# Optimization experiments

Hardware: AMD Instinct MI355X
Metric: run time of the kernel (lower is better)

The kernel has to match this reference:

```python
import jax, jax.numpy as jnp
import numpy as np
import math

B, S, H, NH, NKV, D, I, LCK = 2, 1024, 2048, 32, 8, 64, 8192, 3
EPS = 1e-6
THETA = 10000.0


def rms_norm(x, w, eps=EPS):
    xf = x.astype(jnp.float32)
    var = jnp.mean(xf * xf, axis=-1, keepdims=True)
    return (w * (xf * jax.lax.rsqrt(var + eps))).astype(x.dtype)


def rotate_half(x):
    d = x.shape[-1] // 2
    return jnp.concatenate([-x[..., d:], x[..., :d]], axis=-1)


def setup_inputs() -> dict:
    key = jax.random.key(0)
    ks = jax.random.split(key, 16)
    sc = 0.02
    inp = {
        'input_emb': jax.random.normal(ks[0], (B, S, H), jnp.float32),
        'hidden_states': jax.random.normal(ks[1], (B, S, H), jnp.float32),
        'cache_k': jax.random.normal(ks[2], (LCK, B, NH, S, D), jnp.float32),
        'cache_v': jax.random.normal(ks[3], (LCK, B, NH, S, D), jnp.float32),
    }
    neg = jnp.finfo(jnp.float32).min
    causal = jnp.where(jnp.tril(jnp.ones((S, S), bool)), 0.0, neg).astype(jnp.float32)
    inp['attention_mask'] = jnp.broadcast_to(causal[None, None], (B, 1, S, S))
    inp['position_ids'] = jnp.broadcast_to(jnp.arange(S, dtype=jnp.int32)[None], (B, S))
    inp['wq'] = jax.random.normal(ks[4], (NH * D, 2 * H), jnp.float32) * sc
    inp['wk'] = jax.random.normal(ks[5], (NKV * D, 2 * H), jnp.float32) * sc
    inp['wv'] = jax.random.normal(ks[6], (NKV * D, 2 * H), jnp.float32) * sc
    inp['wo'] = jax.random.normal(ks[7], (H, NH * D), jnp.float32) * sc
    inp['w_gate'] = jax.random.normal(ks[8], (I, H), jnp.float32) * sc
    inp['w_up'] = jax.random.normal(ks[9], (I, H), jnp.float32) * sc
    inp['w_down'] = jax.random.normal(ks[10], (H, I), jnp.float32) * sc
    inp['hidden_norm_w'] = jnp.ones((H,), jnp.float32)
    inp['input_ln_w'] = jnp.ones((H,), jnp.float32)
    inp['post_ln_w'] = jnp.ones((H,), jnp.float32)
    return inp


def _forward(input_emb, hidden_states, cache_k, cache_v, attention_mask, position_ids,
             wq, wk, wv, wo, w_gate, w_up, w_down, hidden_norm_w, input_ln_w, post_ln_w):
    residual = hidden_states
    h = rms_norm(hidden_states, hidden_norm_w)
    e = rms_norm(input_emb, input_ln_w)
    x = jnp.concatenate([e, h], axis=-1)  # [B,S,2H]

    q = jnp.einsum('bsi,oi->bso', x, wq).reshape(B, S, NH, D).transpose(0, 2, 1, 3)
    k = jnp.einsum('bsi,oi->bso', x, wk).reshape(B, S, NKV, D).transpose(0, 2, 1, 3)
    v = jnp.einsum('bsi,oi->bso', x, wv).reshape(B, S, NKV, D).transpose(0, 2, 1, 3)

    # RoPE table up to seq_len = S + LCK, indexed at position_ids + LCK
    inv_freq = 1.0 / (THETA ** (jnp.arange(0, D, 2, dtype=jnp.float32) / D))
    t = jnp.arange(S + LCK, dtype=jnp.float32)
    freqs = t[:, None] * inv_freq[None, :]
    emb = jnp.concatenate([freqs, freqs], axis=-1)  # [S+LCK, D]
    pos = position_ids + LCK
    cos = jnp.cos(emb)[pos][:, None]  # [B,1,S,D]
    sin = jnp.sin(emb)[pos][:, None]
    q = q * cos + rotate_half(q) * sin
    k = k * cos + rotate_half(k) * sin

    n_rep = NH // NKV
    k = jnp.repeat(k, n_rep, axis=1)  # [B,NH,S,D]
    v = jnp.repeat(v, n_rep, axis=1)

    scale = 1.0 / math.sqrt(D)
    # full causal attention against the oldest cache entry
    s0 = jnp.einsum('bhqd,bhkd->bhqk', q, cache_k[0]) * scale + attention_mask
    # diagonal (same-position) attention against remaining cache entries + current keys
    extra_k = jnp.concatenate([cache_k[1:], k[None]], axis=0)  # [LCK,B,NH,S,D]
    extra_v = jnp.concatenate([cache_v[1:], v[None]], axis=0)
    sd = jnp.einsum('bhqd,nbhqd->bhqn', q, extra_k) * scale  # [B,NH,S,LCK]

    attn = jax.nn.softmax(jnp.concatenate([s0, sd], axis=-1).astype(jnp.float32), axis=-1).astype(q.dtype)
    out = jnp.einsum('bhqk,bhkd->bhqd', attn[..., :S], cache_v[0])
    out = out + jnp.einsum('bhqn,nbhqd->bhqd', attn[..., S:], extra_v)
    out = out.transpose(0, 2, 1, 3).reshape(B, S, NH * D)
    attn_out = jnp.einsum('bsi,oi->bso', out, wo)

    h2 = residual + attn_out
    hn = rms_norm(h2, post_ln_w)
    mlp = jnp.einsum('bsi,oi->bso', jax.nn.silu(jnp.einsum('bsi,oi->bso', hn, w_gate)) * jnp.einsum('bsi,oi->bso', hn, w_up), w_down)
    return h2 + mlp


def reference(input_emb, hidden_states, cache_k, cache_v, attention_mask, position_ids,
              wq, wk, wv, wo, w_gate, w_up, w_down, hidden_norm_w, input_ln_w, post_ln_w):
    return _forward(input_emb, hidden_states, cache_k, cache_v, attention_mask, position_ids,
                    wq, wk, wv, wo, w_gate, w_up, w_down, hidden_norm_w, input_ln_w, post_ln_w)
```

## Files before the change

### kernel.cpp

```cpp
#include <hip/hip_runtime.h>
#include <math.h>

#define B_   2
#define S_   1024
#define H_   2048
#define NH_  32
#define NKV_ 8
#define D_   64
#define I_   8192
#define LCK_ 3
#define M_   (B_ * S_)

typedef unsigned short u16;
typedef unsigned int   u32;
typedef __attribute__((ext_vector_type(8))) short bf16x8;
typedef __attribute__((ext_vector_type(4))) float f32x4;
typedef __attribute__((ext_vector_type(2))) unsigned int u32x2;

__device__ __forceinline__ u16 f2b(float f) {
  u32 u = __float_as_uint(f);
  u += 0x7fffu + ((u >> 16) & 1u);
  return (u16)(u >> 16);
}
__device__ __forceinline__ float b2f(u16 h) { return __uint_as_float(((u32)h) << 16); }

__device__ __forceinline__ void st_bf4(u16* p, float a, float b, float c, float d) {
  u32x2 v;
  v.x = (u32)f2b(a) | ((u32)f2b(b) << 16);
  v.y = (u32)f2b(c) | ((u32)f2b(d) << 16);
  *(u32x2*)p = v;
}

__device__ __forceinline__ void cvt16(const float4& a, const float4& b,
                                      const float4& c, const float4& d,
                                      bf16x8& lo, bf16x8& hi) {
  lo[0] = (short)f2b(a.x); lo[1] = (short)f2b(a.y); lo[2] = (short)f2b(a.z); lo[3] = (short)f2b(a.w);
  lo[4] = (short)f2b(b.x); lo[5] = (short)f2b(b.y); lo[6] = (short)f2b(b.z); lo[7] = (short)f2b(b.w);
  hi[0] = (short)f2b(c.x); hi[1] = (short)f2b(c.y); hi[2] = (short)f2b(c.z); hi[3] = (short)f2b(c.w);
  hi[4] = (short)f2b(d.x); hi[5] = (short)f2b(d.y); hi[6] = (short)f2b(d.z); hi[7] = (short)f2b(d.w);
}

__device__ __forceinline__ void async16(const void* g, void* l) {
  __builtin_amdgcn_global_load_lds(
      (const __attribute__((address_space(1))) unsigned int*)(uintptr_t)g,
      (__attribute__((address_space(3))) unsigned int*)(unsigned int)(uintptr_t)l,
      16, 0, 0);
}

__global__ __launch_bounds__(256) void norm_concat_kernel(
    const float* __restrict__ emb, const float* __restrict__ hid,
    const float* __restrict__ w_e, const float* __restrict__ w_h,
    u16* __restrict__ x)
{
  const int row = blockIdx.x;
  const int t = threadIdx.x;
  const float* e = emb + (size_t)row * H_;
  const float* h = hid + (size_t)row * H_;

  const float4 ev0 = *(const float4*)&e[t * 4];
  const float4 ev1 = *(const float4*)&e[t * 4 + 1024];
  const float4 hv0 = *(const float4*)&h[t * 4];
  const float4 hv1 = *(const float4*)&h[t * 4 + 1024];

  float se = ev0.x*ev0.x + ev0.y*ev0.y + ev0.z*ev0.z + ev0.w*ev0.w
           + ev1.x*ev1.x + ev1.y*ev1.y + ev1.z*ev1.z + ev1.w*ev1.w;
  float sh = hv0.x*hv0.x + hv0.y*hv0.y + hv0.z*hv0.z + hv0.w*hv0.w
           + hv1.x*hv1.x + hv1.y*hv1.y + hv1.z*hv1.z + hv1.w*hv1.w;

  #pragma unroll
  for (int m = 1; m < 64; m <<= 1) {
    se += __shfl_xor(se, m);
    sh += __shfl_xor(sh, m);
  }
  __shared__ float red[8];
  const int wv = t >> 6;
  if ((t & 63) == 0) { red[wv] = se; red[4 + wv] = sh; }
  __syncthreads();
  se = red[0] + red[1] + red[2] + red[3];
  sh = red[4] + red[5] + red[6] + red[7];

  const float re = 1.0f / sqrtf(se * (1.0f / H_) + 1e-6f);
  const float rh = 1.0f / sqrtf(sh * (1.0f / H_) + 1e-6f);

  const float4 we0 = *(const float4*)&w_e[t * 4];
  const float4 we1 = *(const float4*)&w_e[t * 4 + 1024];
  const float4 wh0 = *(const float4*)&w_h[t * 4];
  const float4 wh1 = *(const float4*)&w_h[t * 4 + 1024];

  u16* xr = x + (size_t)row * (2 * H_);
  st_bf4(&xr[t * 4],        ev0.x*re*we0.x, ev0.y*re*we0.y, ev0.z*re*we0.z, ev0.w*re*we0.w);
  st_bf4(&xr[t * 4 + 1024], ev1.x*re*we1.x, ev1.y*re*we1.y, ev1.z*re*we1.z, ev1.w*re*we1.w);
  st_bf4(&xr[2048 + t * 4],        hv0.x*rh*wh0.x, hv0.y*rh*wh0.y, hv0.z*rh*wh0.z, hv0.w*rh*wh0.w);
  st_bf4(&xr[2048 + t * 4 + 1024], hv1.x*rh*wh1.x, hv1.y*rh*wh1.y, hv1.z*rh*wh1.z, hv1.w*rh*wh1.w);
}

__global__ __launch_bounds__(256) void rmsnorm_kernel(
    const float* __restrict__ in, const float* __restrict__ w, u16* __restrict__ outp)
{
  const int row = blockIdx.x;
  const int t = threadIdx.x;
  const float* p = in + (size_t)row * H_;
  const float4 v0 = *(const float4*)&p[t * 4];
  const float4 v1 = *(const float4*)&p[t * 4 + 1024];
  float s = v0.x*v0.x + v0.y*v0.y + v0.z*v0.z + v0.w*v0.w
          + v1.x*v1.x + v1.y*v1.y + v1.z*v1.z + v1.w*v1.w;
  #pragma unroll
  for (int m = 1; m < 64; m <<= 1) s += __shfl_xor(s, m);
  __shared__ float red[4];
  const int wv = t >> 6;
  if ((t & 63) == 0) red[wv] = s;
  __syncthreads();
  s = red[0] + red[1] + red[2] + red[3];
  const float rs = 1.0f / sqrtf(s * (1.0f / H_) + 1e-6f);

  const float4 w0 = *(const float4*)&w[t * 4];
  const float4 w1 = *(const float4*)&w[t * 4 + 1024];
  u16* orow = outp + (size_t)row * H_;
  st_bf4(&orow[t * 4],        v0.x*rs*w0.x, v0.y*rs*w0.y, v0.z*rs*w0.z, v0.w*rs*w0.w);
  st_bf4(&orow[t * 4 + 1024], v1.x*rs*w1.x, v1.y*rs*w1.y, v1.z*rs*w1.z, v1.w*rs*w1.w);
}

__global__ __launch_bounds__(256) void convert6_kernel(
    const float* __restrict__ wq, const float* __restrict__ wk, const float* __restrict__ wv,
    const float* __restrict__ wo, const float* __restrict__ wg, const float* __restrict__ wu,
    u16* __restrict__ dst)
{
  const size_t i8 = ((size_t)blockIdx.x * 256 + threadIdx.x) * 8;
  const float* s; size_t base;
  if      (i8 <  8388608) { s = wq; base = 0; }
  else if (i8 < 10485760) { s = wk; base = 8388608; }
  else if (i8 < 12582912) { s = wv; base = 10485760; }
  else if (i8 < 16777216) { s = wo; base = 12582912; }
  else if (i8 < 33554432) { s = wg; base = 16777216; }
  else                    { s = wu; base = 33554432; }
  const float4 a = *(const float4*)&s[i8 - base];
  const float4 b = *(const float4*)&s[i8 - base + 4];
  bf16x8 r;
  r[0] = (short)f2b(a.x); r[1] = (short)f2b(a.y); r[2] = (short)f2b(a.z); r[3] = (short)f2b(a.w);
  r[4] = (short)f2b(b.x); r[5] = (short)f2b(b.y); r[6] = (short)f2b(b.z); r[7] = (short)f2b(b.w);
  *(bf16x8*)&dst[i8] = r;
}

__global__ __launch_bounds__(256) void convert1_kernel(
    const float* __restrict__ src, u16* __restrict__ dst)
{
  const size_t i8 = ((size_t)blockIdx.x * 256 + threadIdx.x) * 8;
  const float4 a = *(const float4*)&src[i8];
  const float4 b = *(const float4*)&src[i8 + 4];
  bf16x8 r;
  r[0] = (short)f2b(a.x); r[1] = (short)f2b(a.y); r[2] = (short)f2b(a.z); r[3] = (short)f2b(a.w);
  r[4] = (short)f2b(b.x); r[5] = (short)f2b(b.y); r[6] = (short)f2b(b.z); r[7] = (short)f2b(b.w);
  *(bf16x8*)&dst[i8] = r;
}

template <int MODE>
__global__ __launch_bounds__(256) void gemm_bf16_kernel(
    const u16* __restrict__ A, const u16* __restrict__ Bw,
    void* Cv, const void* Xv, int M, int N, int K)
{
  __shared__ __align__(16) u16 As[2][128 * 32];
  __shared__ __align__(16) u16 Bs[2][128 * 32];
  const int t = threadIdx.x;
  const int lane = t & 63;
  const int w = t >> 6;
  const int wr = w >> 1, wc = w & 1;
  const int row0 = blockIdx.y * 128;
  const int col0 = blockIdx.x * 128;
  const int kz = blockIdx.z;
  const int Kc = K / (int)gridDim.z;

  f32x4 acc[4][4];
  #pragma unroll
  for (int i = 0; i < 4; ++i)
    #pragma unroll
    for (int j = 0; j < 4; ++j)
      #pragma unroll
      for (int r = 0; r < 4; ++r) acc[i][j][r] = 0.f;

  const int srow = lane >> 2;
  const int skc  = (lane & 3) * 8;
  const u16* Ag = A  + (size_t)(row0 + w * 32 + srow) * K + skc + (size_t)kz * Kc;
  const u16* Bg = Bw + (size_t)(col0 + w * 32 + srow) * K + skc + (size_t)kz * Kc;
  u16* AsW0 = &As[0][w * 32 * 32];
  u16* AsW1 = &As[1][w * 32 * 32];
  u16* BsW0 = &Bs[0][w * 32 * 32];
  u16* BsW1 = &Bs[1][w * 32 * 32];

  const int fr = lane & 15;
  const int fq = (lane >> 4) * 8;

  auto stage = [&](int k0, u16* aw, u16* bw) {
    async16(Ag + k0,                  aw);
    async16(Ag + k0 + (size_t)16 * K, aw + 16 * 32);
    async16(Bg + k0,                  bw);
    async16(Bg + k0 + (size_t)16 * K, bw + 16 * 32);
  };
  auto compute = [&](const u16* asb, const u16* bsb) {
    bf16x8 af[4], bfr[4];
    #pragma unroll
    for (int ti = 0; ti < 4; ++ti)
      af[ti] = *(const bf16x8*)&asb[(wr * 64 + ti * 16 + fr) * 32 + fq];
    #pragma unroll
    for (int tj = 0; tj < 4; ++tj)
      bfr[tj] = *(const bf16x8*)&bsb[(wc * 64 + tj * 16 + fr) * 32 + fq];
    #pragma unroll
    for (int ti = 0; ti < 4; ++ti)
      #pragma unroll
      for (int tj = 0; tj < 4; ++tj)
        acc[ti][tj] = __builtin_amdgcn_mfma_f32_16x16x32_bf16(af[ti], bfr[tj], acc[ti][tj], 0, 0, 0);
  };

  stage(0, AsW0, BsW0);
  __syncthreads();

  int k0 = 0;
  for (;;) {
    if (k0 + 32 < Kc) stage(k0 + 32, AsW1, BsW1);
    compute(As[0], Bs[0]);
    if (k0 + 32 >= Kc) break;
    __syncthreads();
    if (k0 + 64 < Kc) stage(k0 + 64, AsW0, BsW0);
    compute(As[1], Bs[1]);
    if (k0 + 64 >= Kc) break;
    __syncthreads();
    k0 += 64;
  }

  float* Cf = (float*)Cv + (size_t)kz * ((size_t)M * N);
  u16*  Cb = (u16*)Cv;
  const float* Xf = (const float*)Xv;
  const u16*  Xb = (const u16*)Xv;
  const int rbase = (lane >> 4) * 4;
  const int cofs  = lane & 15;
  #pragma unroll
  for (int ti = 0; ti < 4; ++ti) {
    #pragma unroll
    for (int r = 0; r < 4; ++r) {
      const int gr = row0 + wr * 64 + ti * 16 + rbase + r;
      #pragma unroll
      for (int tj = 0; tj < 4; ++tj) {
        const int gc = col0 + wc * 64 + tj * 16 + cofs;
        const size_t off = (size_t)gr * N + gc;
        const float v = acc[ti][tj][r];
        if constexpr (MODE == 0) {
          Cf[off] = v;
        } else if constexpr (MODE == 1) {
          Cf[off] = v + Xf[off];
        } else if constexpr (MODE == 2) {
          Cb[off] = f2b(v);
        } else {
          const float g = b2f(Xb[off]);
          Cb[off] = f2b((g / (1.f + __expf(-g))) * v);
        }
      }
    }
  }
}

template <int NP>
__global__ __launch_bounds__(256) void reduce_kernel(
    const float* __restrict__ p, const float* __restrict__ resid,
    float* __restrict__ out, size_t nper)
{
  const size_t i = ((size_t)blockIdx.x * 256 + threadIdx.x) * 4;
  float4 s = *(const float4*)&p[i];
  #pragma unroll
  for (int z = 1; z < NP; ++z) {
    const float4 a = *(const float4*)&p[(size_t)z * nper + i];
    s.x += a.x; s.y += a.y; s.z += a.z; s.w += a.w;
  }
  if (resid) {
    const float4 r = *(const float4*)&resid[i];
    s.x += r.x; s.y += r.y; s.z += r.z; s.w += r.w;
  }
  *(float4*)&out[i] = s;
}

__global__ __launch_bounds__(256) void rope_kernel(
    float* __restrict__ qkv, const int* __restrict__ pid)
{
  const int idx = blockIdx.x * 256 + threadIdx.x;
  const int total = M_ * (NH_ + NKV_) * 32;
  if (idx >= total) return;
  const int row = idx / 1280;
  const int rem = idx - row * 1280;
  const int head = rem >> 5;
  const int i = rem & 31;
  const int col = (head < NH_) ? head * 64 : 2048 + (head - NH_) * 64;
  float* base = qkv + (size_t)row * 3072 + col;
  const int pos = pid[row] + LCK_;
  const float invf = exp2f((float)i * (-13.2877123795494f / 32.0f));
  const float ang = (float)pos * invf;
  float sn, c;
  __sincosf(ang, &sn, &c);
  const float x0 = base[i];
  const float x1 = base[i + 32];
  base[i]      = x0 * c - x1 * sn;
  base[i + 32] = x1 * c + x0 * sn;
}

__global__ __launch_bounds__(256) void attn_kernel(
    const float* __restrict__ qkv,
    const float* __restrict__ ck, const float* __restrict__ cv,
    u16* __restrict__ ao)
{
  const int bid = blockIdx.x;
  const int qt = bid & 15;
  const int bh = bid >> 4;
  const int h = bh & 31;
  const int b = bh >> 5;
  const int t = threadIdx.x;
  const int lane = t & 63;
  const int w = t >> 6;
  const int qbase = qt * 64;

  const int fr = lane & 15;
  const int fq = (lane >> 4) * 8;
  const int rbase = (lane >> 4) * 4;
  const int cofs = lane & 15;

  __shared__ __align__(16) u16 Qs[64 * 72];
  __shared__ __align__(16) u16 Ks[64 * 72];
  __shared__ __align__(16) u16 Vts[64 * 72];
  __shared__ __align__(16) u16 Ps[64 * 72];
  __shared__ float Ls[192];

  const size_t bh_off = (size_t)b * NH_ + h;
  const float* K0 = ck + bh_off * S_ * D_;
  const float* V0 = cv + bh_off * S_ * D_;

  const int sr = t >> 2;
  const int sc = (t & 3) * 16;
  {
    const float* qg = qkv + (size_t)(b * S_ + qbase + sr) * 3072 + h * 64 + sc;
    float4 a = *(const float4*)&qg[0], bb = *(const float4*)&qg[4],
           c = *(const float4*)&qg[8], d = *(const float4*)&qg[12];
    a.x*=0.125f; a.y*=0.125f; a.z*=0.125f; a.w*=0.125f;
    bb.x*=0.125f; bb.y*=0.125f; bb.z*=0.125f; bb.w*=0.125f;
    c.x*=0.125f; c.y*=0.125f; c.z*=0.125f; c.w*=0.125f;
    d.x*=0.125f; d.y*=0.125f; d.z*=0.125f; d.w*=0.125f;
    bf16x8 lo, hi; cvt16(a, bb, c, d, lo, hi);
    *(bf16x8*)&Qs[sr * 72 + sc] = lo;
    *(bf16x8*)&Qs[sr * 72 + sc + 8] = hi;
  }

  float m_r[4], l_r[4];
  f32x4 Oacc[4];
  #pragma unroll
  for (int r = 0; r < 4; ++r) { m_r[r] = -3.0e38f; l_r[r] = 0.f; }
  #pragma unroll
  for (int dt = 0; dt < 4; ++dt)
    #pragma unroll
    for (int r = 0; r < 4; ++r) Oacc[dt][r] = 0.f;

  for (int kt = 0; kt <= qt; ++kt) {
    __syncthreads();
    {
      const float* kg = K0 + (size_t)(kt * 64 + sr) * D_ + sc;
      float4 a = *(const float4*)&kg[0], bb = *(const float4*)&kg[4],
             c = *(const float4*)&kg[8], d = *(const float4*)&kg[12];
      bf16x8 lo, hi; cvt16(a, bb, c, d, lo, hi);
      *(bf16x8*)&Ks[sr * 72 + sc] = lo;
      *(bf16x8*)&Ks[sr * 72 + sc + 8] = hi;
      const float* vg = V0 + (size_t)(kt * 64 + sr) * D_ + sc;
      float4 va = *(const float4*)&vg[0], vb4 = *(const float4*)&vg[4],
             vc = *(const float4*)&vg[8], vd = *(const float4*)&vg[12];
      const float vv[16] = {va.x,va.y,va.z,va.w, vb4.x,vb4.y,vb4.z,vb4.w,
                            vc.x,vc.y,vc.z,vc.w, vd.x,vd.y,vd.z,vd.w};
      #pragma unroll
      for (int i = 0; i < 16; ++i) Vts[(sc + i) * 72 + sr] = f2b(vv[i]);
    }
    __syncthreads();

    const bf16x8 qa0 = *(const bf16x8*)&Qs[(w * 16 + fr) * 72 + fq];
    const bf16x8 qa1 = *(const bf16x8*)&Qs[(w * 16 + fr) * 72 + 32 + fq];
    f32x4 sacc[4];
    #pragma unroll
    for (int nt = 0; nt < 4; ++nt) {
      const bf16x8 kb0 = *(const bf16x8*)&Ks[(nt * 16 + fr) * 72 + fq];
      const bf16x8 kb1 = *(const bf16x8*)&Ks[(nt * 16 + fr) * 72 + 32 + fq];
      f32x4 z; z[0]=0.f; z[1]=0.f; z[2]=0.f; z[3]=0.f;
      z = __builtin_amdgcn_mfma_f32_16x16x32_bf16(qa0, kb0, z, 0, 0, 0);
      sacc[nt] = __builtin_amdgcn_mfma_f32_16x16x32_bf16(qa1, kb1, z, 0, 0, 0);
    }
    if (kt == qt) {
      #pragma unroll
      for (int nt = 0; nt < 4; ++nt) {
        const int key = nt * 16 + cofs;
        #pragma unroll
        for (int r = 0; r < 4; ++r)
          if (key > w * 16 + rbase + r) sacc[nt][r] = -3.0e38f;
      }
    }

    #pragma unroll
    for (int r = 0; r < 4; ++r) {
      float rm = fmaxf(fmaxf(sacc[0][r], sacc[1][r]), fmaxf(sacc[2][r], sacc[3][r]));
      rm = fmaxf(rm, __shfl_xor(rm, 1));
      rm = fmaxf(rm, __shfl_xor(rm, 2));
      rm = fmaxf(rm, __shfl_xor(rm, 4));
      rm = fmaxf(rm, __shfl_xor(rm, 8));
      const float mnew = fmaxf(m_r[r], rm);
      const float alpha = __expf(m_r[r] - mnew);
      float p0 = __expf(sacc[0][r] - mnew);
      float p1 = __expf(sacc[1][r] - mnew);
      float p2 = __expf(sacc[2][r] - mnew);
      float p3 = __expf(sacc[3][r] - mnew);
      float rs = p0 + p1 + p2 + p3;
      rs += __shfl_xor(rs, 1);
      rs += __shfl_xor(rs, 2);
      rs += __shfl_xor(rs, 4);
      rs += __shfl_xor(rs, 8);
      l_r[r] = l_r[r] * alpha + rs;
      m_r[r] = mnew;
      #pragma unroll
      for (int dt = 0; dt < 4; ++dt) Oacc[dt][r] *= alpha;
      u16* prow = &Ps[(w * 16 + rbase + r) * 72 + cofs];
      prow[0]  = f2b(p0);
      prow[16] = f2b(p1);
      prow[32] = f2b(p2);
      prow[48] = f2b(p3);
    }

    const bf16x8 pa0 = *(const bf16x8*)&Ps[(w * 16 + fr) * 72 + fq];
    const bf16x8 pa1 = *(const bf16x8*)&Ps[(w * 16 + fr) * 72 + 32 + fq];
    #pragma unroll
    for (int dt = 0; dt < 4; ++dt) {
      const bf16x8 vb0 = *(const bf16x8*)&Vts[(dt * 16 + fr) * 72 + fq];
      const bf16x8 vb1 = *(const bf16x8*)&Vts[(dt * 16 + fr) * 72 + 32 + fq];
      Oacc[dt] = __builtin_amdgcn_mfma_f32_16x16x32_bf16(pa0, vb0, Oacc[dt], 0, 0, 0);
      Oacc[dt] = __builtin_amdgcn_mfma_f32_16x16x32_bf16(pa1, vb1, Oacc[dt], 0, 0, 0);
    }
  }

  if (t < 192) {
    const int n = t >> 6;
    const int r = t & 63;
    const int qp = qbase + r;
    const float* kp;
    if (n < 2) kp = ck + ((((size_t)(n + 1) * B_ + b) * NH_ + h) * S_ + qp) * D_;
    else       kp = qkv + (size_t)(b * S_ + qp) * 3072 + 2048 + (h >> 2) * 64;
    float e = 0.f;
    #pragma unroll 16
    for (int d = 0; d < 64; ++d) e = fmaf(b2f(Qs[r * 72 + d]), kp[d], e);
    Ls[n * 64 + r] = e;
  }
  __syncthreads();

  #pragma unroll
  for (int r = 0; r < 4; ++r) {
    const int qr = w * 16 + rbase + r;
    const int qp = qbase + qr;
    const float e0 = Ls[qr], e1 = Ls[64 + qr], e2 = Ls[128 + qr];
    const float mnew = fmaxf(fmaxf(m_r[r], e0), fmaxf(e1, e2));
    const float alpha = __expf(m_r[r] - mnew);
    const float p0 = __expf(e0 - mnew);
    const float p1 = __expf(e1 - mnew);
    const float p2 = __expf(e2 - mnew);
    const float inv = 1.0f / (l_r[r] * alpha + p0 + p1 + p2);
    const float* v1p = cv + ((((size_t)1 * B_ + b) * NH_ + h) * S_ + qp) * D_;
    const float* v2p = cv + ((((size_t)2 * B_ + b) * NH_ + h) * S_ + qp) * D_;
    const float* v3p = qkv + (size_t)(b * S_ + qp) * 3072 + 2560 + (h >> 2) * 64;
    u16* aorow = ao + (size_t)(b * S_ + qp) * 2048 + h * 64;
    #pragma unroll
    for (int dt = 0; dt < 4; ++dt) {
      const int col = dt * 16 + cofs;
      const float o = (Oacc[dt][r] * alpha + p0 * v1p[col] + p1 * v2p[col] + p2 * v3p[col]) * inv;
      aorow[col] = f2b(o);
    }
  }
}

extern "C" void kernel_launch(void* const* d_in, const int* in_sizes, int n_in,
                              void* d_out, int out_size, void* d_ws, size_t ws_size,
                              hipStream_t stream)
{
  const float* input_emb = (const float*)d_in[0];
  const float* hidden    = (const float*)d_in[1];
  const float* cache_k   = (const float*)d_in[2];
  const float* cache_v   = (const float*)d_in[3];
  const int*   pos_ids   = (const int*)d_in[5];
  const float* wq = (const float*)d_in[6];
  const float* wk = (const float*)d_in[7];
  const float* wv = (const float*)d_in[8];
  const float* wo = (const float*)d_in[9];
  const float* wg = (const float*)d_in[10];
  const float* wu = (const float*)d_in[11];
  const float* wd = (const float*)d_in[12];
  const float* w_hidden_norm = (const float*)d_in[13];
  const float* w_input_ln    = (const float*)d_in[14];
  const float* w_post_ln     = (const float*)d_in[15];
  float* out = (float*)d_out;

  char* wsb = (char*)d_ws;
  u16*   wall   = (u16*)(wsb + 0);
  u16*   wqkv_b = wall;
  u16*   wo_b   = (u16*)(wsb + 25165824);
  u16*   wg_b   = (u16*)(wsb + 33554432);
  u16*   wu_b   = (u16*)(wsb + 67108864);
  u16*   xb     = (u16*)(wsb + 100663296);
  float* qkvf   = (float*)(wsb + 117440512);
  u16*   ao     = (u16*)(wsb + 142606336);
  float* h2     = (float*)(wsb + 150994944);
  u16*   hn     = (u16*)(wsb + 100663296);
  u16*   gbb    = (u16*)(wsb + 117440512);
  u16*   gub    = (u16*)(wsb + 0);
  u16*   wd_b   = (u16*)(wsb + 33554432);
  float* wo_p   = (float*)(wsb + 100663296);
  float* dn_p   = (float*)(wsb + 67108864);

  convert6_kernel<<<24576, 256, 0, stream>>>(wq, wk, wv, wo, wg, wu, wall);
  norm_concat_kernel<<<M_, 256, 0, stream>>>(input_emb, hidden, w_input_ln, w_hidden_norm, xb);
  gemm_bf16_kernel<0><<<dim3(24, 16, 2), 256, 0, stream>>>(xb, wqkv_b, qkvf, nullptr, M_, 3072, 4096);
  reduce_kernel<2><<<6144, 256, 0, stream>>>(qkvf, nullptr, qkvf, (size_t)M_ * 3072);
  rope_kernel<<<10240, 256, 0, stream>>>(qkvf, pos_ids);
  attn_kernel<<<B_ * NH_ * (S_ / 64), 256, 0, stream>>>(qkvf, cache_k, cache_v, ao);
  gemm_bf16_kernel<0><<<dim3(16, 16, 2), 256, 0, stream>>>(ao, wo_b, wo_p, nullptr, M_, 2048, 2048);
  reduce_kernel<2><<<4096, 256, 0, stream>>>(wo_p, hidden, h2, (size_t)M_ * 2048);
  rmsnorm_kernel<<<M_, 256, 0, stream>>>(h2, w_post_ln, hn);
  gemm_bf16_kernel<2><<<dim3(64, 16), 256, 0, stream>>>(hn, wg_b, gbb, nullptr, M_, 8192, 2048);
  convert1_kernel<<<8192, 256, 0, stream>>>(wd, wd_b);
  gemm_bf16_kernel<3><<<dim3(64, 16), 256, 0, stream>>>(hn, wu_b, gub, gbb, M_, 8192, 2048);
  gemm_bf16_kernel<0><<<dim3(16, 16, 4), 256, 0, stream>>>(gub, wd_b, dn_p, nullptr, M_, 2048, 8192);
  reduce_kernel<4><<<4096, 256, 0, stream>>>(dn_p, h2, out, (size_t)M_ * 2048);
}
```

Measured before the change: 929.7 us.

## Deepen GEMM LDS pipeline to four stages with explicit vmcnt waits

```diff
diff --git a/kernel.cpp b/kernel.cpp
--- a/kernel.cpp
+++ b/kernel.cpp
@@ -158,8 +158,8 @@
     const u16* __restrict__ A, const u16* __restrict__ Bw,
     void* Cv, const void* Xv, int M, int N, int K)
 {
-  __shared__ __align__(16) u16 As[2][128 * 32];
-  __shared__ __align__(16) u16 Bs[2][128 * 32];
+  __shared__ __align__(16) u16 As[4][128 * 32];
+  __shared__ __align__(16) u16 Bs[4][128 * 32];
   const int t = threadIdx.x;
   const int lane = t & 63;
   const int w = t >> 6;
@@ -168,6 +168,7 @@
   const int col0 = blockIdx.x * 128;
   const int kz = blockIdx.z;
   const int Kc = K / (int)gridDim.z;
+  const int nsteps = Kc >> 5;
 
   f32x4 acc[4][4];
   #pragma unroll
@@ -181,19 +182,16 @@
   const int skc  = (lane & 3) * 8;
   const u16* Ag = A  + (size_t)(row0 + w * 32 + srow) * K + skc + (size_t)kz * Kc;
   const u16* Bg = Bw + (size_t)(col0 + w * 32 + srow) * K + skc + (size_t)kz * Kc;
-  u16* AsW0 = &As[0][w * 32 * 32];
-  u16* AsW1 = &As[1][w * 32 * 32];
-  u16* BsW0 = &Bs[0][w * 32 * 32];
-  u16* BsW1 = &Bs[1][w * 32 * 32];
+  const int wofs = w * 1024;
 
   const int fr = lane & 15;
   const int fq = (lane >> 4) * 8;
 
-  auto stage = [&](int k0, u16* aw, u16* bw) {
-    async16(Ag + k0,                  aw);
-    async16(Ag + k0 + (size_t)16 * K, aw + 16 * 32);
-    async16(Bg + k0,                  bw);
-    async16(Bg + k0 + (size_t)16 * K, bw + 16 * 32);
+  auto stageTo = [&](int k0, u16* ab, u16* bb) {
+    async16(Ag + k0,                  ab + wofs);
+    async16(Ag + k0 + (size_t)16 * K, ab + wofs + 512);
+    async16(Bg + k0,                  bb + wofs);
+    async16(Bg + k0 + (size_t)16 * K, bb + wofs + 512);
   };
   auto compute = [&](const u16* asb, const u16* bsb) {
     bf16x8 af[4], bfr[4];
@@ -210,20 +208,23 @@
         acc[ti][tj] = __builtin_amdgcn_mfma_f32_16x16x32_bf16(af[ti], bfr[tj], acc[ti][tj], 0, 0, 0);
   };
 
-  stage(0, AsW0, BsW0);
-  __syncthreads();
-
-  int k0 = 0;
-  for (;;) {
-    if (k0 + 32 < Kc) stage(k0 + 32, AsW1, BsW1);
-    compute(As[0], Bs[0]);
-    if (k0 + 32 >= Kc) break;
-    __syncthreads();
-    if (k0 + 64 < Kc) stage(k0 + 64, AsW0, BsW0);
-    compute(As[1], Bs[1]);
-    if (k0 + 64 >= Kc) break;
-    __syncthreads();
-    k0 += 64;
+  u16 *A0 = &As[0][0], *A1 = &As[1][0], *A2 = &As[2][0], *A3 = &As[3][0];
+  u16 *B0 = &Bs[0][0], *B1 = &Bs[1][0], *B2 = &Bs[2][0], *B3 = &Bs[3][0];
+
+  stageTo(0,  A0, B0);
+  stageTo(32, A1, B1);
+  stageTo(64, A2, B2);
+
+  for (int kt = 0; kt < nsteps; ++kt) {
+    const int rem = nsteps - 1 - kt;
+    if (rem >= 2)      asm volatile("s_waitcnt vmcnt(8) lgkmcnt(0)" ::: "memory");
+    else if (rem == 1) asm volatile("s_waitcnt vmcnt(4) lgkmcnt(0)" ::: "memory");
+    else               asm volatile("s_waitcnt vmcnt(0) lgkmcnt(0)" ::: "memory");
+    __builtin_amdgcn_s_barrier();
+    if (kt + 3 < nsteps) stageTo((kt + 3) * 32, A3, B3);
+    compute(A0, B0);
+    u16* ta = A0; A0 = A1; A1 = A2; A2 = A3; A3 = ta;
+    u16* tb = B0; B0 = B1; B1 = B2; B2 = B3; B3 = tb;
   }
 
   float* Cf = (float*)Cv + (size_t)kz * ((size_t)M * N);
```

New measurement: 878.6 us. -5.5%, faster.
